# Optimization experiments

Hardware: AMD Instinct MI355X
Metric: run time of the kernel (lower is better)

Reference implementation:

```python
import jax, jax.numpy as jnp
import numpy as np

D_MODEL = 1024
NUM_HEADS = 16


def setup_inputs() -> dict:
    key = jax.random.key(0)
    ks = jax.random.split(key, 5)
    scale = 1.0 / np.sqrt(D_MODEL)
    X = jax.random.normal(ks[0], (4, 2048, D_MODEL), dtype=jnp.float32)
    W_q = jax.random.normal(ks[1], (D_MODEL, D_MODEL), dtype=jnp.float32) * scale
    W_k = jax.random.normal(ks[2], (D_MODEL, D_MODEL), dtype=jnp.float32) * scale
    W_v = jax.random.normal(ks[3], (D_MODEL, D_MODEL), dtype=jnp.float32) * scale
    W_o = jax.random.normal(ks[4], (D_MODEL, D_MODEL), dtype=jnp.float32) * scale
    return {"X": X, "W_q": W_q, "W_k": W_k, "W_v": W_v, "W_o": W_o}


def reference(X, W_q, W_k, W_v, W_o):
    b, s, d_model = X.shape
    h = NUM_HEADS
    d_k = d_model // h
    # Linear projections (y = x @ W^T convention; W stored as [out,in] would be
    # x @ W.T, but with random weights we use x @ W — math is identical in form).
    def split_heads(y):
        return y.reshape(b, s, h, d_k).transpose(0, 2, 1, 3)  # b h s d
    q = split_heads(X @ W_q)
    k = split_heads(X @ W_k)
    v = split_heads(X @ W_v)
    scores = jnp.einsum('bhid,bhjd->bhij', q, k) / jnp.sqrt(jnp.float32(d_k))
    causal = jnp.tril(jnp.ones((s, s), dtype=bool))
    scores = jnp.where(causal[None, None], scores, jnp.float32(-jnp.inf))
    probs = jax.nn.softmax(scores, axis=-1)
    attended = jnp.einsum('bhij,bhjd->bhid', probs, v)
    out = attended.transpose(0, 2, 1, 3).reshape(b, s, d_model)
    return out @ W_o
```

## Files before the change

kernel.cpp:

```cpp
#include <hip/hip_runtime.h>

typedef __bf16 bf16;
typedef __attribute__((ext_vector_type(8))) __bf16 bf16x8;
typedef __attribute__((ext_vector_type(4))) float f32x4;
typedef __attribute__((ext_vector_type(16))) float f32x16;
typedef __attribute__((ext_vector_type(4))) unsigned short u16x4;
typedef __attribute__((ext_vector_type(2))) int v2i;

#define D_MODEL 1024
#define SEQ     2048
#define NB      4
#define NH      16
#define DK      64
#define MROWS   (NB * SEQ)

#define MFMA_BF16 __builtin_amdgcn_mfma_f32_16x16x32_bf16
#define MFMA32    __builtin_amdgcn_mfma_f32_32x32x16_bf16
#define EXP2F(x) __builtin_amdgcn_exp2f(x)
#define QSCALE 0.18033688011112042f

#define BARRIER() do { asm volatile("" ::: "memory"); \
                       __builtin_amdgcn_s_barrier();  \
                       asm volatile("" ::: "memory"); } while (0)

__device__ __forceinline__ bf16 f2b(float f) {
    union { float f; unsigned u; } c; c.f = f;
    unsigned r = (c.u + 0x7fffu + ((c.u >> 16) & 1u)) >> 16;
    union { unsigned short s; bf16 b; } o; o.s = (unsigned short)r;
    return o.b;
}
__device__ __forceinline__ unsigned short f2u(float f) {
    union { float f; unsigned u; } c; c.f = f;
    return (unsigned short)((c.u + 0x7fffu + ((c.u >> 16) & 1u)) >> 16);
}

__device__ __forceinline__ f32x16 zero16() {
    f32x16 z = {0.f,0.f,0.f,0.f,0.f,0.f,0.f,0.f,
                0.f,0.f,0.f,0.f,0.f,0.f,0.f,0.f};
    return z;
}

template <int N> struct IC { static constexpr int v = N; };

__global__ void prep_kernel(const float* __restrict__ X,
                            const float* __restrict__ Wq, const float* __restrict__ Wk,
                            const float* __restrict__ Wv, const float* __restrict__ Wo,
                            bf16* __restrict__ Xb, bf16* __restrict__ WqkvT,
                            bf16* __restrict__ WoT) {
    __shared__ float tile[32][33];
    const int bid = blockIdx.x;
    if (bid < 8192) {
        int i = bid * 256 + threadIdx.x;
        float4 v = ((const float4*)X)[i];
        u16x4 o; o[0] = f2u(v.x); o[1] = f2u(v.y); o[2] = f2u(v.z); o[3] = f2u(v.w);
        ((u16x4*)Xb)[i] = o;
    } else {
        int r = bid - 8192;
        int w = r >> 10, tl = r & 1023;
        const float* src = (w == 0) ? Wq : (w == 1) ? Wk : (w == 2) ? Wv : Wo;
        bf16* dst = (w == 3) ? WoT : WqkvT + (size_t)w * 1024 * 1024;
        const int n0 = (tl & 31) * 32, k0 = (tl >> 5) * 32;
        const int tx = threadIdx.x & 31, ty = threadIdx.x >> 5;
#pragma unroll
        for (int i = 0; i < 4; i++)
            tile[ty + i * 8][tx] = src[(size_t)(k0 + ty + i * 8) * 1024 + n0 + tx];
        __syncthreads();
#pragma unroll
        for (int i = 0; i < 4; i++)
            dst[(size_t)(n0 + ty + i * 8) * 1024 + k0 + tx] = f2b(tile[tx][ty + i * 8]);
    }
}

__global__ __launch_bounds__(512, 2) void gemm_qkv(const bf16* __restrict__ A,
                                                   const bf16* __restrict__ Bt,
                                                   bf16* __restrict__ outQ,
                                                   bf16* __restrict__ outV) {
    __shared__ __align__(16) char lds[98304];

    const int t = threadIdx.x;
    const int wid = t >> 6, lane = t & 63;
    const int ln = lane & 15, qd = lane >> 4;
    const int wm = wid >> 1, wn = wid & 1;
    const int swk = ln & 7;

    const int wg = (blockIdx.x & 7) * 96 + (blockIdx.x >> 3);
    const int rowb = wg & 31, colb = wg >> 5;
    const int row0 = rowb * 256, col0 = colb * 128;
    const bool isQK = (col0 < 2048);

    const int srow = t >> 3;
    const int schunk = (t & 7) ^ (srow & 7);
    const bf16* ga = A  + (size_t)(row0 + srow) * 1024 + schunk * 8;
    const bf16* gb = Bt + (size_t)(col0 + srow) * 1024 + schunk * 8;

    auto stageA = [&](int kt, int buf) {
#pragma unroll
        for (int c = 0; c < 4; c++)
            __builtin_amdgcn_global_load_lds(
                (const __attribute__((address_space(1))) void*)
                    (ga + (size_t)(c * 64) * 1024 + kt * 64),
                (__attribute__((address_space(3))) void*)
                    (lds + buf * 32768 + c * 8192 + t * 16), 16, 0, 0);
    };
    auto stageB = [&](int kt, int buf) {
#pragma unroll
        for (int c = 0; c < 2; c++)
            __builtin_amdgcn_global_load_lds(
                (const __attribute__((address_space(1))) void*)
                    (gb + (size_t)(c * 64) * 1024 + kt * 64),
                (__attribute__((address_space(3))) void*)
                    (lds + 65536 + buf * 16384 + c * 8192 + t * 16), 16, 0, 0);
    };

    const char* pABase = lds + (wm * 64 + ln) * 128;
    const char* pBBase = lds + 65536 + (wn * 64 + ln) * 128;
    const int cks0 = (qd ^ swk) * 16;
    const int cks1 = ((4 + qd) ^ swk) * 16;

    f32x4 acc[4][4];
#pragma unroll
    for (int i = 0; i < 4; i++)
#pragma unroll
        for (int j = 0; j < 4; j++) acc[i][j] = (f32x4){0.f, 0.f, 0.f, 0.f};

    stageA(0, 0); stageB(0, 0);
    stageA(1, 1); stageB(1, 1);
    asm volatile("s_waitcnt vmcnt(6)" ::: "memory");
    BARRIER();

    auto ktile = [&](auto bufc, int kt) {
        constexpr int BUF = decltype(bufc)::v;
        const char* pa0 = pABase + BUF * 32768 + cks0;
        const char* pa1 = pABase + BUF * 32768 + cks1;
        const char* pb0 = pBBase + BUF * 16384 + cks0;
        const char* pb1 = pBBase + BUF * 16384 + cks1;

        bf16x8 af[4][2], bfr[4][2];
#pragma unroll
        for (int i = 0; i < 4; i++) {
            af[i][0] = *(const bf16x8*)(pa0 + i * 2048);
            af[i][1] = *(const bf16x8*)(pa1 + i * 2048);
        }
#pragma unroll
        for (int j = 0; j < 4; j++) {
            bfr[j][0] = *(const bf16x8*)(pb0 + j * 2048);
            bfr[j][1] = *(const bf16x8*)(pb1 + j * 2048);
        }
        asm volatile("s_waitcnt lgkmcnt(0)" ::: "memory");
        __builtin_amdgcn_sched_barrier(0);
        BARRIER();

        __builtin_amdgcn_s_setprio(1);
        if (isQK) {
#pragma unroll
            for (int i = 0; i < 4; i++)
#pragma unroll
                for (int j = 0; j < 4; j++)
                    acc[i][j] = MFMA_BF16(bfr[j][0], af[i][0], acc[i][j], 0, 0, 0);
        } else {
#pragma unroll
            for (int i = 0; i < 4; i++)
#pragma unroll
                for (int j = 0; j < 4; j++)
                    acc[i][j] = MFMA_BF16(af[i][0], bfr[j][0], acc[i][j], 0, 0, 0);
        }
        __builtin_amdgcn_s_setprio(0);

        if (kt + 2 < 16) { stageA(kt + 2, BUF); stageB(kt + 2, BUF); }

        __builtin_amdgcn_s_setprio(1);
        if (isQK) {
#pragma unroll
            for (int i = 0; i < 4; i++)
#pragma unroll
                for (int j = 0; j < 4; j++)
                    acc[i][j] = MFMA_BF16(bfr[j][1], af[i][1], acc[i][j], 0, 0, 0);
        } else {
#pragma unroll
            for (int i = 0; i < 4; i++)
#pragma unroll
                for (int j = 0; j < 4; j++)
                    acc[i][j] = MFMA_BF16(af[i][1], bfr[j][1], acc[i][j], 0, 0, 0);
        }
        __builtin_amdgcn_s_setprio(0);

        if (kt + 2 < 16) {
            asm volatile("s_waitcnt vmcnt(6)" ::: "memory");
        } else if (kt + 1 < 16) {
            asm volatile("s_waitcnt vmcnt(0)" ::: "memory");
        }
        BARRIER();
    };

#pragma unroll 1
    for (int kt = 0; kt < 16; kt += 2) {
        ktile(IC<0>{}, kt);
        ktile(IC<1>{}, kt + 1);
    }

    if (isQK) {
#pragma unroll
        for (int i = 0; i < 4; i++)
#pragma unroll
            for (int j = 0; j < 4; j++) {
                int m  = row0 + wm * 64 + i * 16 + ln;
                int n0 = col0 + wn * 64 + j * 16 + qd * 4;
                float scale = (n0 < 1024) ? QSCALE : 1.0f;
                int b = m >> 11, s = m & 2047;
                int h = (n0 & 1023) >> 6, d0 = n0 & 63;
                size_t addr = (((size_t)(b * NH + h) * SEQ + s) * DK + d0)
                              + (size_t)(n0 >> 10) * 8388608;
                u16x4 w;
#pragma unroll
                for (int r = 0; r < 4; r++) w[r] = f2u(acc[i][j][r] * scale);
                *(u16x4*)&outQ[addr] = w;
            }
    } else {
#pragma unroll
        for (int i = 0; i < 4; i++)
#pragma unroll
            for (int j = 0; j < 4; j++) {
                int m0 = row0 + wm * 64 + i * 16 + qd * 4;
                int n  = col0 + wn * 64 + j * 16 + ln - 2048;
                int b = m0 >> 11, s0 = m0 & 2047;
                int h = n >> 6, d = n & 63;
                size_t addr = ((size_t)(b * NH + h) * DK + d) * SEQ + s0;
                u16x4 w;
#pragma unroll
                for (int r = 0; r < 4; r++) w[r] = f2u(acc[i][j][r]);
                *(u16x4*)&outV[addr] = w;
            }
    }
}

__global__ __launch_bounds__(256) void gemm_o(const bf16* __restrict__ A,
                                              const bf16* __restrict__ Bt,
                                              float* __restrict__ out) {
    __shared__ __align__(16) bf16 lA[128 * 64];
    __shared__ __align__(16) bf16 lB[128 * 64];

    const int t = threadIdx.x;
    const int wid = t >> 6, lane = t & 63;
    const int ln = lane & 15, qd = lane >> 4;
    const int wm = wid >> 1, wn = wid & 1;

    const int bid = blockIdx.x;
    const int colb = bid & 7, rowb = bid >> 3;
    const int row0 = rowb * 128, col0 = colb * 128;

    const int srow = t >> 3;
    const int schunk = (t & 7) ^ (srow & 7);
    const bf16* ga = A  + (size_t)(row0 + srow) * 1024 + schunk * 8;
    const bf16* gb = Bt + (size_t)(col0 + srow) * 1024 + schunk * 8;
    const int swk = ln & 7;

    f32x4 acc[4][4];
#pragma unroll
    for (int i = 0; i < 4; i++)
#pragma unroll
        for (int j = 0; j < 4; j++) acc[i][j] = (f32x4){0.f, 0.f, 0.f, 0.f};

    for (int kb = 0; kb < 1024; kb += 64) {
#pragma unroll
        for (int c = 0; c < 4; c++) {
            __builtin_amdgcn_global_load_lds(
                (const __attribute__((address_space(1))) void*)(ga + kb + (size_t)c * 32 * 1024),
                (__attribute__((address_space(3))) void*)(&lA[t * 8 + c * 2048]), 16, 0, 0);
            __builtin_amdgcn_global_load_lds(
                (const __attribute__((address_space(1))) void*)(gb + kb + (size_t)c * 32 * 1024),
                (__attribute__((address_space(3))) void*)(&lB[t * 8 + c * 2048]), 16, 0, 0);
        }
        __syncthreads();

#pragma unroll
        for (int ks = 0; ks < 2; ks++) {
            bf16x8 af[4], bfr[4];
#pragma unroll
            for (int i = 0; i < 4; i++)
                af[i] = *(const bf16x8*)&lA[(wm * 64 + i * 16 + ln) * 64
                                            + ((ks * 4 + qd) ^ swk) * 8];
#pragma unroll
            for (int j = 0; j < 4; j++)
                bfr[j] = *(const bf16x8*)&lB[(wn * 64 + j * 16 + ln) * 64
                                             + ((ks * 4 + qd) ^ swk) * 8];
#pragma unroll
            for (int i = 0; i < 4; i++)
#pragma unroll
                for (int j = 0; j < 4; j++)
                    acc[i][j] = MFMA_BF16(bfr[j], af[i], acc[i][j], 0, 0, 0);
        }
        __syncthreads();
    }

#pragma unroll
    for (int i = 0; i < 4; i++)
#pragma unroll
        for (int j = 0; j < 4; j++) {
            int m  = row0 + wm * 64 + i * 16 + ln;
            int n0 = col0 + wn * 64 + j * 16 + qd * 4;
            *(f32x4*)&out[(size_t)m * 1024 + n0] = acc[i][j];
        }
}

__global__ __launch_bounds__(128, 2) void attn_kernel(const bf16* __restrict__ Q,
                                                      const bf16* __restrict__ K,
                                                      const bf16* __restrict__ Vt,
                                                      bf16* __restrict__ attn_out) {
    __shared__ __align__(16) bf16 smem[4][64 * 64];

    const int t = threadIdx.x;
    const int wid = t >> 6, lane = t & 63;
    const int qcol = lane & 31, h = lane >> 5;

    const int bid = blockIdx.x;
    const int bh = ((bid >> 7) << 3) | (bid & 7);
    const int p  = (bid >> 3) & 15;
    const int gA = 31 - p, gB = p;
    const int ntA = gA + 1;

    const bf16* Qh = Q  + (size_t)bh * SEQ * DK;
    const bf16* Kh = K  + (size_t)bh * SEQ * DK;
    const bf16* Vh = Vt + (size_t)bh * DK * SEQ;

    const int srow = t >> 3;
    const int schunk = (t & 7) ^ (srow & 7);
    const bf16* kgp = Kh + (size_t)srow * DK + schunk * 8;
    const bf16* vgp = Vh + (size_t)srow * SEQ + schunk * 8;

    const char* sbase = (const char*)&smem[0][0];
    int raddr[4];
#pragma unroll
    for (int tt = 0; tt < 4; tt++)
        raddr[tt] = qcol * 128 + (((2 * tt + h) ^ (lane & 7)) * 16);

    int qw0;
    bf16x8 qf[4];
    f32x16 o[2];
    float l;

    auto initGroup = [&](int g) {
        qw0 = g * 64 + wid * 32;
#pragma unroll
        for (int tt = 0; tt < 4; tt++)
            qf[tt] = *(const bf16x8*)(Qh + (size_t)(qw0 + qcol) * DK + tt * 16 + h * 8);
        o[0] = zero16(); o[1] = zero16();
        l = 0.f;
    };

    const int b = bh >> 4, head = bh & 15;
    auto finalize = [&]() {
        float ll = l + __shfl_xor(l, 32);
        const float inv = 1.0f / ll;
        const size_t orow = ((size_t)(b * SEQ + qw0 + qcol)) * D_MODEL + head * DK;
#pragma unroll
        for (int m = 0; m < 2; m++)
#pragma unroll
            for (int q4 = 0; q4 < 4; q4++) {
                u16x4 w;
#pragma unroll
                for (int c = 0; c < 4; c++) w[c] = f2u(o[m][q4 * 4 + c] * inv);
                *(u16x4*)&attn_out[orow + m * 32 + q4 * 8 + h * 4] = w;
            }
    };

    auto stage = [&](int kb, int buf) {
#pragma unroll
        for (int c = 0; c < 4; c++) {
            __builtin_amdgcn_global_load_lds(
                (const __attribute__((address_space(1))) void*)(kgp + (size_t)(kb + c * 16) * DK),
                (__attribute__((address_space(3))) void*)(&smem[buf][t * 8 + c * 1024]), 16, 0, 0);
            __builtin_amdgcn_global_load_lds(
                (const __attribute__((address_space(1))) void*)(vgp + (size_t)c * 16 * SEQ + kb),
                (__attribute__((address_space(3))) void*)(&smem[2 + buf][t * 8 + c * 1024]), 16, 0, 0);
        }
    };

    auto qkt = [&](const char* kb_base) -> f32x16 {
        f32x16 z = zero16();
#pragma unroll
        for (int tt = 0; tt < 4; tt++) {
            bf16x8 kf = *(const bf16x8*)(kb_base + raddr[tt]);
            z = MFMA32(kf, qf[tt], z, 0, 0, 0);
        }
        return z;
    };

    auto pvks = [&](const f32x16& s, int b8, int ks, const char* vbase) {
        unsigned A, B, C, D;
        asm("v_cvt_pk_bf16_f32 %0, %1, %2"
            : "=v"(A) : "v"(s[b8 + 0]), "v"(s[b8 + 1]));
        asm("v_cvt_pk_bf16_f32 %0, %1, %2"
            : "=v"(B) : "v"(s[b8 + 2]), "v"(s[b8 + 3]));
        asm("v_cvt_pk_bf16_f32 %0, %1, %2"
            : "=v"(C) : "v"(s[b8 + 4]), "v"(s[b8 + 5]));
        asm("v_cvt_pk_bf16_f32 %0, %1, %2"
            : "=v"(D) : "v"(s[b8 + 6]), "v"(s[b8 + 7]));
        v2i r02 = __builtin_amdgcn_permlane32_swap((int)A, (int)C, false, false);
        v2i r13 = __builtin_amdgcn_permlane32_swap((int)B, (int)D, false, false);
        union { unsigned u[4]; bf16x8 v; } pf;
        pf.u[0] = (unsigned)r02[0];
        pf.u[1] = (unsigned)r13[0];
        pf.u[2] = (unsigned)r02[1];
        pf.u[3] = (unsigned)r13[1];
#pragma unroll
        for (int m = 0; m < 2; m++) {
            bf16x8 vf = *(const bf16x8*)(vbase + raddr[ks] + m * 4096);
            o[m] = MFMA32(vf, pf.v, o[m], 0, 0, 0);
        }
    };

    auto smaxFull = [&](f32x16& s) -> float {
#pragma unroll
        for (int r = 0; r < 16; r++) s[r] = EXP2F(s[r]);
        float s0 = (s[0] + s[1]) + (s[2] + s[3]);
        float s1 = (s[4] + s[5]) + (s[6] + s[7]);
        float s2 = (s[8] + s[9]) + (s[10] + s[11]);
        float s3 = (s[12] + s[13]) + (s[14] + s[15]);
        return (s0 + s1) + (s2 + s3);
    };

    auto compute = [&](auto curc, int kb) {
        constexpr int CUR = decltype(curc)::v;
        const char* kbase = sbase + CUR * 8192;
        const char* vbase = sbase + 16384 + CUR * 8192;
        const int rel = qw0 - kb;
        if (rel < 0) return;
        if (rel >= 64) {
            __builtin_amdgcn_s_setprio(1);
            f32x16 s0 = qkt(kbase);
            f32x16 s1 = qkt(kbase + 4096);
            __builtin_amdgcn_s_setprio(0);
            l += smaxFull(s0);
            __builtin_amdgcn_s_setprio(1);
            pvks(s0, 0, 0, vbase);
            pvks(s0, 8, 1, vbase);
            __builtin_amdgcn_s_setprio(0);
            l += smaxFull(s1);
            __builtin_amdgcn_s_setprio(1);
            pvks(s1, 0, 2, vbase);
            pvks(s1, 8, 3, vbase);
            __builtin_amdgcn_s_setprio(0);
        } else {
            const int nt = (rel >> 5) + 1;
            f32x16 st[2];
#pragma unroll
            for (int n = 0; n < 2; n++)
                if (n < nt) st[n] = qkt(kbase + n * 4096);
            float ps = 0.f;
#pragma unroll
            for (int n = 0; n < 2; n++)
                if (n < nt) {
                    const bool diag = (rel == 32 * n);
#pragma unroll
                    for (int r = 0; r < 16; r++) {
                        float pv = EXP2F(st[n][r]);
                        if (diag) {
                            const int kloc = (r & 3) + 8 * (r >> 2) + 4 * h;
                            pv = (kloc > qcol) ? 0.f : pv;
                        }
                        st[n][r] = pv;
                    }
                    float s0 = (st[n][0] + st[n][1]) + (st[n][2] + st[n][3]);
                    float s1 = (st[n][4] + st[n][5]) + (st[n][6] + st[n][7]);
                    float s2 = (st[n][8] + st[n][9]) + (st[n][10] + st[n][11]);
                    float s3 = (st[n][12] + st[n][13]) + (st[n][14] + st[n][15]);
                    ps += (s0 + s1) + (s2 + s3);
                }
            l += ps;
#pragma unroll
            for (int ks = 0; ks < 4; ks++)
                if (ks < 2 * nt)
                    pvks(st[ks >> 1], (ks & 1) * 8, ks, vbase);
        }
    };

    auto step = [&](auto curc, int i) {
        constexpr int CUR = decltype(curc)::v;
        __syncthreads();
        const int nx = i + 1;
        if (nx < 33) {
            const int tnx = (nx < ntA) ? nx : nx - ntA;
            stage(tnx * 64, CUR ^ 1);
        }
        const int kb = ((i < ntA) ? i : i - ntA) * 64;
        compute(curc, kb);
        if (i == ntA - 1) { finalize(); initGroup(gB); }
    };

    stage(0, 0);
    initGroup(gA);

    step(IC<0>{}, 0);
#pragma unroll 1
    for (int ii = 0; ii < 16; ii++) {
        step(IC<1>{}, 2 * ii + 1);
        step(IC<0>{}, 2 * ii + 2);
    }
    finalize();
}

extern "C" void kernel_launch(void* const* d_in, const int* in_sizes, int n_in,
                              void* d_out, int out_size, void* d_ws, size_t ws_size,
                              hipStream_t stream) {
    const float* X  = (const float*)d_in[0];
    const float* Wq = (const float*)d_in[1];
    const float* Wk = (const float*)d_in[2];
    const float* Wv = (const float*)d_in[3];
    const float* Wo = (const float*)d_in[4];
    float* out = (float*)d_out;
    char* ws = (char*)d_ws;

    bf16* Xb    = (bf16*)(ws);
    bf16* WqkvT = (bf16*)(ws + (16u << 20));
    bf16* WoT   = (bf16*)(ws + (22u << 20));
    bf16* Qb    = (bf16*)(ws + (24u << 20));
    bf16* Vt    = (bf16*)(ws + (56u << 20));
    bf16* Attn  = Xb;
    bf16* Kb    = Qb + (size_t)8388608;

    prep_kernel<<<dim3(12288), dim3(256), 0, stream>>>(X, Wq, Wk, Wv, Wo,
                                                       Xb, WqkvT, WoT);

    gemm_qkv<<<dim3(768), dim3(512), 0, stream>>>(Xb, WqkvT, Qb, Vt);

    attn_kernel<<<dim3(1024), dim3(128), 0, stream>>>(Qb, Kb, Vt, Attn);

    gemm_o<<<dim3(512), dim3(256), 0, stream>>>(Attn, WoT, out);
}
```

Before: 253.0 us.

## Split GEMM k-tile into four interleaved phases with staggered LDS prefetch

Restructures the projection GEMM main loop so that each k-tile runs as four smaller phases. Each phase reads a subset of the A/B fragments from LDS, issues part of the next tile's global-to-LDS copy (A halves and B split across phases), and runs eight MFMAs. Previously a k-tile did one large fragment load and two 16-MFMA bursts. The aim is to spread global-load issue and LDS reads across the MFMA work for finer-grained overlap and lower register pressure for fragments. The cost is many more workgroup barriers per k-tile and a more delicate vmcnt accounting, which could add sync stalls.

```diff
diff --git a/kernel.cpp b/kernel.cpp
--- a/kernel.cpp
+++ b/kernel.cpp
@@ -93,15 +93,24 @@
     const bf16* ga = A  + (size_t)(row0 + srow) * 1024 + schunk * 8;
     const bf16* gb = Bt + (size_t)(col0 + srow) * 1024 + schunk * 8;
 
-    auto stageA = [&](int kt, int buf) {
-#pragma unroll
-        for (int c = 0; c < 4; c++)
+    auto stageA0 = [&](int kt, int buf) {
+#pragma unroll
+        for (int c = 0; c < 2; c++)
             __builtin_amdgcn_global_load_lds(
                 (const __attribute__((address_space(1))) void*)
                     (ga + (size_t)(c * 64) * 1024 + kt * 64),
                 (__attribute__((address_space(3))) void*)
                     (lds + buf * 32768 + c * 8192 + t * 16), 16, 0, 0);
     };
+    auto stageA1 = [&](int kt, int buf) {
+#pragma unroll
+        for (int c = 2; c < 4; c++)
+            __builtin_amdgcn_global_load_lds(
+                (const __attribute__((address_space(1))) void*)
+                    (ga + (size_t)(c * 64) * 1024 + kt * 64),
+                (__attribute__((address_space(3))) void*)
+                    (lds + buf * 32768 + c * 8192 + t * 16), 16, 0, 0);
+    };
     auto stageB = [&](int kt, int buf) {
 #pragma unroll
         for (int c = 0; c < 2; c++)
@@ -123,9 +132,9 @@
 #pragma unroll
         for (int j = 0; j < 4; j++) acc[i][j] = (f32x4){0.f, 0.f, 0.f, 0.f};
 
-    stageA(0, 0); stageB(0, 0);
-    stageA(1, 1); stageB(1, 1);
-    asm volatile("s_waitcnt vmcnt(6)" ::: "memory");
+    stageA0(0, 0); stageA1(0, 0); stageB(0, 0);
+    stageA0(1, 1);
+    asm volatile("s_waitcnt vmcnt(2)" ::: "memory");
     BARRIER();
 
     auto ktile = [&](auto bufc, int kt) {
@@ -135,57 +144,61 @@
         const char* pb0 = pBBase + BUF * 16384 + cks0;
         const char* pb1 = pBBase + BUF * 16384 + cks1;
 
-        bf16x8 af[4][2], bfr[4][2];
-#pragma unroll
-        for (int i = 0; i < 4; i++) {
-            af[i][0] = *(const bf16x8*)(pa0 + i * 2048);
-            af[i][1] = *(const bf16x8*)(pa1 + i * 2048);
-        }
-#pragma unroll
-        for (int j = 0; j < 4; j++) {
-            bfr[j][0] = *(const bf16x8*)(pb0 + j * 2048);
-            bfr[j][1] = *(const bf16x8*)(pb1 + j * 2048);
-        }
+        bf16x8 af[4], bf01[2], bf23[2];
+
+        auto mfma8 = [&](const bf16x8 (&bp)[2], int j0) {
+            __builtin_amdgcn_s_setprio(1);
+            if (isQK) {
+#pragma unroll
+                for (int i = 0; i < 4; i++)
+#pragma unroll
+                    for (int j = 0; j < 2; j++)
+                        acc[i][j0 + j] = MFMA_BF16(bp[j], af[i], acc[i][j0 + j], 0, 0, 0);
+            } else {
+#pragma unroll
+                for (int i = 0; i < 4; i++)
+#pragma unroll
+                    for (int j = 0; j < 2; j++)
+                        acc[i][j0 + j] = MFMA_BF16(af[i], bp[j], acc[i][j0 + j], 0, 0, 0);
+            }
+            __builtin_amdgcn_s_setprio(0);
+        };
+
+#pragma unroll
+        for (int i = 0; i < 4; i++) af[i] = *(const bf16x8*)(pa0 + i * 2048);
+#pragma unroll
+        for (int j = 0; j < 2; j++) bf01[j] = *(const bf16x8*)(pb0 + j * 2048);
+        if (kt + 1 < 16) stageA1(kt + 1, BUF ^ 1);
+        BARRIER();
         asm volatile("s_waitcnt lgkmcnt(0)" ::: "memory");
-        __builtin_amdgcn_sched_barrier(0);
-        BARRIER();
-
-        __builtin_amdgcn_s_setprio(1);
-        if (isQK) {
-#pragma unroll
-            for (int i = 0; i < 4; i++)
-#pragma unroll
-                for (int j = 0; j < 4; j++)
-                    acc[i][j] = MFMA_BF16(bfr[j][0], af[i][0], acc[i][j], 0, 0, 0);
-        } else {
-#pragma unroll
-            for (int i = 0; i < 4; i++)
-#pragma unroll
-                for (int j = 0; j < 4; j++)
-                    acc[i][j] = MFMA_BF16(af[i][0], bfr[j][0], acc[i][j], 0, 0, 0);
-        }
-        __builtin_amdgcn_s_setprio(0);
-
-        if (kt + 2 < 16) { stageA(kt + 2, BUF); stageB(kt + 2, BUF); }
-
-        __builtin_amdgcn_s_setprio(1);
-        if (isQK) {
-#pragma unroll
-            for (int i = 0; i < 4; i++)
-#pragma unroll
-                for (int j = 0; j < 4; j++)
-                    acc[i][j] = MFMA_BF16(bfr[j][1], af[i][1], acc[i][j], 0, 0, 0);
-        } else {
-#pragma unroll
-            for (int i = 0; i < 4; i++)
-#pragma unroll
-                for (int j = 0; j < 4; j++)
-                    acc[i][j] = MFMA_BF16(af[i][1], bfr[j][1], acc[i][j], 0, 0, 0);
-        }
-        __builtin_amdgcn_s_setprio(0);
-
+        mfma8(bf01, 0);
+        BARRIER();
+
+#pragma unroll
+        for (int j = 0; j < 2; j++) bf23[j] = *(const bf16x8*)(pb0 + (2 + j) * 2048);
+        if (kt + 1 < 16) stageB(kt + 1, BUF ^ 1);
+        BARRIER();
+        asm volatile("s_waitcnt lgkmcnt(0)" ::: "memory");
+        mfma8(bf23, 2);
+        BARRIER();
+
+#pragma unroll
+        for (int i = 0; i < 4; i++) af[i] = *(const bf16x8*)(pa1 + i * 2048);
+#pragma unroll
+        for (int j = 0; j < 2; j++) bf01[j] = *(const bf16x8*)(pb1 + j * 2048);
+        BARRIER();
+        asm volatile("s_waitcnt lgkmcnt(0)" ::: "memory");
+        mfma8(bf01, 0);
+        BARRIER();
+
+#pragma unroll
+        for (int j = 0; j < 2; j++) bf23[j] = *(const bf16x8*)(pb1 + (2 + j) * 2048);
+        if (kt + 2 < 16) stageA0(kt + 2, BUF);
+        BARRIER();
+        asm volatile("s_waitcnt lgkmcnt(0)" ::: "memory");
+        mfma8(bf23, 2);
         if (kt + 2 < 16) {
-            asm volatile("s_waitcnt vmcnt(6)" ::: "memory");
+            asm volatile("s_waitcnt vmcnt(2)" ::: "memory");
         } else if (kt + 1 < 16) {
             asm volatile("s_waitcnt vmcnt(0)" ::: "memory");
         }
```

Measured after the change: 251.6 us. No clear change (-0.6%).
